# Kernel tuning notes

Hardware: AMD Instinct MI355X
Metric: run time of the kernel (lower is better)

The kernel has to match this reference:

```python
import jax, jax.numpy as jnp
import numpy as np

B, S, D_MODEL, N_HEADS, HEAD_DIM = 4, 2048, 1024, 16, 64
NEG = -1e9


def apply_rope_real(x, cos_f, sin_f):
    # x: [B, H, S, D]; cos_f/sin_f: [S, D//2] broadcast over B, H
    x_even = x[..., ::2]
    x_odd = x[..., 1::2]
    out_even = x_even * cos_f - x_odd * sin_f
    out_odd = x_even * sin_f + x_odd * cos_f
    return jnp.stack([out_even, out_odd], axis=-1).reshape(x.shape)


def setup_inputs() -> dict:
    key = jax.random.key(0)
    ks = jax.random.split(key, 8)
    x = jax.random.normal(ks[0], (B, S, D_MODEL), dtype=jnp.float32)
    # RoPE tables: theta_i = 10000^{-2i/d}, angles = pos * theta
    inv_freq = 1.0 / (10000.0 ** (jnp.arange(0, HEAD_DIM, 2, dtype=jnp.float32) / HEAD_DIM))
    angles = jnp.arange(S, dtype=jnp.float32)[:, None] * inv_freq[None, :]  # [S, D/2]
    cos_freqs = jnp.cos(angles)
    sin_freqs = jnp.sin(angles)
    causal_mask = jnp.where(jnp.tril(jnp.ones((S, S), dtype=bool)), 0.0, NEG).astype(jnp.float32)
    scale = 0.02
    w_q = jax.random.normal(ks[1], (D_MODEL, D_MODEL), dtype=jnp.float32) * scale
    w_k = jax.random.normal(ks[2], (D_MODEL, D_MODEL), dtype=jnp.float32) * scale
    w_v = jax.random.normal(ks[3], (D_MODEL, D_MODEL), dtype=jnp.float32) * scale
    w_o = jax.random.normal(ks[4], (D_MODEL, D_MODEL), dtype=jnp.float32) * scale
    return {"x": x, "cos_freqs": cos_freqs, "sin_freqs": sin_freqs,
            "causal_mask": causal_mask, "w_q": w_q, "w_k": w_k, "w_v": w_v, "w_o": w_o}


def reference(x, cos_freqs, sin_freqs, causal_mask, w_q, w_k, w_v, w_o):
    batch, seq_len, _ = x.shape
    scale = 1.0 / jnp.sqrt(jnp.float32(HEAD_DIM))
    # torch Linear: y = x @ W.T
    def proj(w):
        return (x @ w.T).reshape(batch, seq_len, N_HEADS, HEAD_DIM).transpose(0, 2, 1, 3)
    q = apply_rope_real(proj(w_q), cos_freqs, sin_freqs)
    k = apply_rope_real(proj(w_k), cos_freqs, sin_freqs)
    v = proj(w_v)
    attn = jnp.einsum('bhqd,bhkd->bhqk', q, k) * scale + causal_mask
    attn = jax.nn.softmax(attn, axis=-1)
    out = jnp.einsum('bhqk,bhkd->bhqd', attn, v)
    out = out.transpose(0, 2, 1, 3).reshape(batch, seq_len, -1)
    return out @ w_o.T
```

## Files before the change

kernel.cpp:

```cpp
#include <hip/hip_runtime.h>
#include <stdint.h>

#define B_  4
#define S_  2048
#define DM_ 1024
#define NH_ 16
#define HD_ 64

typedef unsigned short ushort_t;
typedef __bf16 bf16x8 __attribute__((ext_vector_type(8)));
typedef float  floatx4 __attribute__((ext_vector_type(4)));
typedef float  floatx16 __attribute__((ext_vector_type(16)));

__device__ __forceinline__ float bf2f(ushort_t u) {
    union { unsigned int i; float f; } v; v.i = ((unsigned int)u) << 16; return v.f;
}
__device__ __forceinline__ ushort_t f2bf(float f) {
    union { float f; unsigned int i; } v; v.f = f;
    unsigned int x = v.i;
    return (ushort_t)((x + 0x7fffu + ((x >> 16) & 1u)) >> 16);
}
__device__ __forceinline__ unsigned int pack_bf16_trunc(float lo, float hi) {
    union { float f; unsigned int u; } a, b;
    a.f = lo; b.f = hi;
    return __builtin_amdgcn_perm(b.u, a.u, 0x07060302u);
}

__global__ __launch_bounds__(256) void cvt_all_kernel(
    const float* __restrict__ x,  const float* __restrict__ wq,
    const float* __restrict__ wk, const float* __restrict__ wv,
    const float* __restrict__ wo,
    ushort_t* __restrict__ xb,  ushort_t* __restrict__ wqb,
    ushort_t* __restrict__ wkb, ushort_t* __restrict__ wvb,
    ushort_t* __restrict__ wob)
{
    const int blk = blockIdx.x;
    const float* src; ushort_t* dst; int off;
    if (blk < 8192)       { src = x;  dst = xb;  off = blk; }
    else if (blk < 9216)  { src = wq; dst = wqb; off = blk - 8192; }
    else if (blk < 10240) { src = wk; dst = wkb; off = blk - 9216; }
    else if (blk < 11264) { src = wv; dst = wvb; off = blk - 10240; }
    else                  { src = wo; dst = wob; off = blk - 11264; }
    const int i = off * 256 + threadIdx.x;
    float4 v = ((const float4*)src)[i];
    ushort4 o; o.x = f2bf(v.x); o.y = f2bf(v.y); o.z = f2bf(v.z); o.w = f2bf(v.w);
    ((ushort4*)dst)[i] = o;
}

__global__ __launch_bounds__(512, 2) void gemm_bt_kernel(
    const ushort_t* __restrict__ A,
    const ushort_t* __restrict__ B0, const ushort_t* __restrict__ B1,
    const ushort_t* __restrict__ B2,
    void* __restrict__ C0, void* __restrict__ C1, void* __restrict__ C2,
    int M, int N, int K, int mode, int nz)
{
    __shared__ ushort_t As[2][16384];
    __shared__ ushort_t Bs[2][8192];

    const int lid = blockIdx.x;
    const int cpx = gridDim.x >> 3;
    const int wg  = (lid & 7) * cpx + (lid >> 3);
    const int x   = wg / (8 * nz);
    const int rr  = wg - x * (8 * nz);
    const int y   = rr & 7;
    const int z   = rr >> 3;

    const ushort_t* Bw = z == 0 ? B0 : z == 1 ? B1 : B2;
    void* Cv           = z == 0 ? C0 : z == 1 ? C1 : C2;

    const int tid  = threadIdx.x;
    const int wave = tid >> 6, lane = tid & 63;
    const int l15 = lane & 15, quad = lane >> 4;
    const int wr = wave >> 1, wc = wave & 1;
    const int mbase = x * 256;
    const int nbase = y * 128;
    const int NT = K >> 6;

    auto stageA = [&](int bt, int t, int L0) {
#pragma unroll
        for (int L = L0; L < L0 + 2; ++L) {
            const int e8  = L * 512 + tid;
            const int row = e8 >> 3, c = e8 & 7;
            const ushort_t* src = A + (size_t)(mbase + row) * K + t * 64 + ((c ^ (row & 7)) << 3);
            __builtin_amdgcn_global_load_lds(
                (const __attribute__((address_space(1))) unsigned int*)src,
                (__attribute__((address_space(3))) unsigned int*)(&As[bt][e8 * 8]), 16, 0, 0);
        }
    };
    auto stageB = [&](int bt, int t, int L) {
        const int e8  = L * 512 + tid;
        const int row = e8 >> 3, c = e8 & 7;
        const ushort_t* src = Bw + (size_t)(nbase + row) * K + t * 64 + ((c ^ (row & 7)) << 3);
        __builtin_amdgcn_global_load_lds(
            (const __attribute__((address_space(1))) unsigned int*)src,
            (__attribute__((address_space(3))) unsigned int*)(&Bs[bt][e8 * 8]), 16, 0, 0);
    };

    floatx4 acc[4][4] = {};

    stageA(0, 0, 0); stageA(0, 0, 2);
    stageB(0, 0, 0); stageB(0, 0, 1);
    if (NT > 1) {
        stageB(1, 1, 0); stageB(1, 1, 1);
        asm volatile("s_waitcnt vmcnt(2)" ::: "memory");
    } else {
        asm volatile("s_waitcnt vmcnt(0)" ::: "memory");
    }
    __builtin_amdgcn_s_barrier();

    auto do_tile = [&](int t, int bt) {
        bf16x8 a0[2][2], a1[2][2], b0[2][2], b1[2][2];
#pragma unroll
        for (int kk = 0; kk < 2; ++kk) {
#pragma unroll
            for (int f = 0; f < 2; ++f) {
                const int row = wr * 64 + f * 16 + l15;
                a0[kk][f] = *(const bf16x8*)&As[bt][row * 64 + ((((kk << 2) | quad)) ^ (l15 & 7)) * 8];
            }
#pragma unroll
            for (int g = 0; g < 2; ++g) {
                const int row = wc * 64 + g * 16 + l15;
                b0[kk][g] = *(const bf16x8*)&Bs[bt][row * 64 + ((((kk << 2) | quad)) ^ (l15 & 7)) * 8];
            }
        }
        if (t + 1 < NT) stageA(bt ^ 1, t + 1, 0);
        __builtin_amdgcn_s_barrier();
        asm volatile("s_waitcnt lgkmcnt(0)" ::: "memory");
        __builtin_amdgcn_s_setprio(1);
#pragma unroll
        for (int kk = 0; kk < 2; ++kk)
#pragma unroll
            for (int mt = 0; mt < 2; ++mt)
#pragma unroll
                for (int nt = 0; nt < 2; ++nt)
                    acc[mt][nt] = __builtin_amdgcn_mfma_f32_16x16x32_bf16(
                        a0[kk][mt], b0[kk][nt], acc[mt][nt], 0, 0, 0);
        __builtin_amdgcn_s_setprio(0);
        __builtin_amdgcn_s_barrier();

#pragma unroll
        for (int kk = 0; kk < 2; ++kk)
#pragma unroll
            for (int g = 0; g < 2; ++g) {
                const int row = wc * 64 + 32 + g * 16 + l15;
                b1[kk][g] = *(const bf16x8*)&Bs[bt][row * 64 + ((((kk << 2) | quad)) ^ (l15 & 7)) * 8];
            }
        if (t + 1 < NT) stageA(bt ^ 1, t + 1, 2);
        __builtin_amdgcn_s_barrier();
        asm volatile("s_waitcnt lgkmcnt(0)" ::: "memory");
        __builtin_amdgcn_s_setprio(1);
#pragma unroll
        for (int kk = 0; kk < 2; ++kk)
#pragma unroll
            for (int mt = 0; mt < 2; ++mt)
#pragma unroll
                for (int nt = 0; nt < 2; ++nt)
                    acc[mt][2 + nt] = __builtin_amdgcn_mfma_f32_16x16x32_bf16(
                        a0[kk][mt], b1[kk][nt], acc[mt][2 + nt], 0, 0, 0);
        __builtin_amdgcn_s_setprio(0);
        __builtin_amdgcn_s_barrier();

#pragma unroll
        for (int kk = 0; kk < 2; ++kk)
#pragma unroll
            for (int f = 0; f < 2; ++f) {
                const int row = wr * 64 + 32 + f * 16 + l15;
                a1[kk][f] = *(const bf16x8*)&As[bt][row * 64 + ((((kk << 2) | quad)) ^ (l15 & 7)) * 8];
            }
        if (t + 2 < NT) stageB(bt, t + 2, 0);
        __builtin_amdgcn_s_barrier();
        asm volatile("s_waitcnt lgkmcnt(0)" ::: "memory");
        __builtin_amdgcn_s_setprio(1);
#pragma unroll
        for (int kk = 0; kk < 2; ++kk)
#pragma unroll
            for (int mt = 0; mt < 2; ++mt)
#pragma unroll
                for (int nt = 0; nt < 2; ++nt)
                    acc[2 + mt][2 + nt] = __builtin_amdgcn_mfma_f32_16x16x32_bf16(
                        a1[kk][mt], b1[kk][nt], acc[2 + mt][2 + nt], 0, 0, 0);
        __builtin_amdgcn_s_setprio(0);
        __builtin_amdgcn_s_barrier();

        if (t + 2 < NT) stageB(bt, t + 2, 1);
        __builtin_amdgcn_s_barrier();
        __builtin_amdgcn_s_setprio(1);
#pragma unroll
        for (int kk = 0; kk < 2; ++kk)
#pragma unroll
            for (int mt = 0; mt < 2; ++mt)
#pragma unroll
                for (int nt = 0; nt < 2; ++nt)
                    acc[2 + mt][nt] = __builtin_amdgcn_mfma_f32_16x16x32_bf16(
                        a1[kk][mt], b0[kk][nt], acc[2 + mt][nt], 0, 0, 0);
        __builtin_amdgcn_s_setprio(0);
        if (t + 2 < NT) { asm volatile("s_waitcnt vmcnt(2)" ::: "memory"); }
        else            { asm volatile("s_waitcnt vmcnt(0)" ::: "memory"); }
        __builtin_amdgcn_s_barrier();
    };

    for (int t = 0; t < NT; t += 2) {
        do_tile(t, 0);
        do_tile(t + 1, 1);
    }

    const bool vtmode = (mode == 0) && (z == 2);
#pragma unroll
    for (int mt = 0; mt < 4; ++mt) {
#pragma unroll
        for (int nt = 0; nt < 4; ++nt) {
            const int col = nbase + wc * 64 + nt * 16 + l15;
            const int m0  = mbase + wr * 64 + mt * 16 + quad * 4;
            if (vtmode) {
                const int b = m0 >> 11, s = m0 & 2047;
                const int hh = col >> 6, d = col & 63;
                uint2 pk;
                pk.x = (unsigned)f2bf(acc[mt][nt][0]) | ((unsigned)f2bf(acc[mt][nt][1]) << 16);
                pk.y = (unsigned)f2bf(acc[mt][nt][2]) | ((unsigned)f2bf(acc[mt][nt][3]) << 16);
                *(uint2*)&((ushort_t*)Cv)[((size_t)((b * NH_ + hh) * HD_ + d)) * S_ + s] = pk;
            } else if (mode == 0) {
#pragma unroll
                for (int r = 0; r < 4; ++r) {
                    const int m = m0 + r;
                    const int b = m >> 11, s = m & 2047;
                    const int hh = col >> 6, d = col & 63;
                    ((ushort_t*)Cv)[(((size_t)(b * NH_ + hh)) * S_ + s) * HD_ + d] =
                        f2bf(acc[mt][nt][r]);
                }
            } else {
#pragma unroll
                for (int r = 0; r < 4; ++r)
                    ((float*)Cv)[(size_t)(m0 + r) * N + col] = acc[mt][nt][r];
            }
        }
    }
}

#define QSCALE 0.1803368801f
__global__ __launch_bounds__(256) void rope_kernel(
    ushort_t* __restrict__ q, ushort_t* __restrict__ k,
    const float* __restrict__ cf, const float* __restrict__ sf)
{
    const int idx = blockIdx.x * 256 + threadIdx.x;
    const int j = idx & 31;
    const int s = (idx >> 5) & (S_ - 1);
    const float c  = cf[s * 32 + j];
    const float sn = sf[s * 32 + j];
    const size_t base = (size_t)idx * 2;
    float qe = bf2f(q[base]), qo = bf2f(q[base + 1]);
    q[base]     = f2bf((qe * c - qo * sn) * QSCALE);
    q[base + 1] = f2bf((qe * sn + qo * c) * QSCALE);
    float ke = bf2f(k[base]), ko = bf2f(k[base + 1]);
    k[base]     = f2bf(ke * c - ko * sn);
    k[base + 1] = f2bf(ke * sn + ko * c);
}

__global__ __launch_bounds__(256, 4) void attn_kernel(
    const ushort_t* __restrict__ Qg, const ushort_t* __restrict__ Kg,
    const ushort_t* __restrict__ Vg, ushort_t* __restrict__ Og)
{
    __shared__ ushort_t Ks[2][64 * 64];
    __shared__ ushort_t Vt[2][64 * 64];

    const int id   = blockIdx.x;
    const int sg   = id >> 3;
    const int bh   = (id & 7) * 8 + (sg & 7);
    const int qtile = 15 - (sg >> 3);
    const int tid  = threadIdx.x;
    const int wave = tid >> 6, lane = tid & 63;
    const int l31 = lane & 31, h = lane >> 5;

    const size_t bh_off = (size_t)bh * S_ * HD_;
    const int b_out = bh >> 4, h_out = bh & 15;

    const int e0 = tid, e1 = tid + 256;
    const int r0 = e0 >> 3, c0 = (e0 & 7) ^ (r0 & 7);
    const int r1 = e1 >> 3, c1 = (e1 & 7) ^ (r1 & 7);

    const int qbase = qtile * 128;
    const int nkt   = 2 * qtile + 2;
    const int qrow  = qbase + wave * 32 + l31;

    bf16x8 qf[4];
#pragma unroll
    for (int ks = 0; ks < 4; ++ks)
        qf[ks] = *(const bf16x8*)(Qg + bh_off + (size_t)qrow * HD_ + ks * 16 + h * 8);

    float m_run = -1e30f, l_run = 0.f;
    floatx16 o_acc[2] = {};

    {
        const ushort_t* ka = Kg + bh_off + (size_t)r0 * HD_ + c0 * 8;
        const ushort_t* kb = Kg + bh_off + (size_t)r1 * HD_ + c1 * 8;
        const ushort_t* va = Vg + bh_off + (size_t)r0 * S_ + c0 * 8;
        const ushort_t* vb = Vg + bh_off + (size_t)r1 * S_ + c1 * 8;
        __builtin_amdgcn_global_load_lds(
            (const __attribute__((address_space(1))) unsigned int*)ka,
            (__attribute__((address_space(3))) unsigned int*)(&Ks[0][e0 * 8]), 16, 0, 0);
        __builtin_amdgcn_global_load_lds(
            (const __attribute__((address_space(1))) unsigned int*)kb,
            (__attribute__((address_space(3))) unsigned int*)(&Ks[0][e1 * 8]), 16, 0, 0);
        __builtin_amdgcn_global_load_lds(
            (const __attribute__((address_space(1))) unsigned int*)va,
            (__attribute__((address_space(3))) unsigned int*)(&Vt[0][e0 * 8]), 16, 0, 0);
        __builtin_amdgcn_global_load_lds(
            (const __attribute__((address_space(1))) unsigned int*)vb,
            (__attribute__((address_space(3))) unsigned int*)(&Vt[0][e1 * 8]), 16, 0, 0);
    }
    asm volatile("s_waitcnt vmcnt(0)" ::: "memory");
    __syncthreads();

    for (int kt = 0; kt < nkt; ++kt) {
        const int kbase = kt * 64;
        const int cur = kt & 1;

        if (kt + 1 < nkt) {
            const int nb = kbase + 64;
            const ushort_t* ka = Kg + bh_off + (size_t)(nb + r0) * HD_ + c0 * 8;
            const ushort_t* kb = Kg + bh_off + (size_t)(nb + r1) * HD_ + c1 * 8;
            const ushort_t* va = Vg + bh_off + (size_t)r0 * S_ + nb + c0 * 8;
            const ushort_t* vb = Vg + bh_off + (size_t)r1 * S_ + nb + c1 * 8;
            __builtin_amdgcn_global_load_lds(
                (const __attribute__((address_space(1))) unsigned int*)ka,
                (__attribute__((address_space(3))) unsigned int*)(&Ks[cur ^ 1][e0 * 8]), 16, 0, 0);
            __builtin_amdgcn_global_load_lds(
                (const __attribute__((address_space(1))) unsigned int*)kb,
                (__attribute__((address_space(3))) unsigned int*)(&Ks[cur ^ 1][e1 * 8]), 16, 0, 0);
            __builtin_amdgcn_global_load_lds(
                (const __attribute__((address_space(1))) unsigned int*)va,
                (__attribute__((address_space(3))) unsigned int*)(&Vt[cur ^ 1][e0 * 8]), 16, 0, 0);
            __builtin_amdgcn_global_load_lds(
                (const __attribute__((address_space(1))) unsigned int*)vb,
                (__attribute__((address_space(3))) unsigned int*)(&Vt[cur ^ 1][e1 * 8]), 16, 0, 0);
        }

        if (kbase <= qbase + wave * 32 + 31) {
            floatx16 st[2] = {};
#pragma unroll
            for (int nt = 0; nt < 2; ++nt) {
                const int krow = nt * 32 + l31;
#pragma unroll
                for (int ks = 0; ks < 4; ++ks) {
                    bf16x8 kf = *(const bf16x8*)&Ks[cur][krow * 64 +
                                    (((ks * 2 + h) ^ (l31 & 7)) << 3)];
                    st[nt] = __builtin_amdgcn_mfma_f32_32x32x16_bf16(kf, qf[ks], st[nt], 0, 0, 0);
                }
            }
            if (kbase + 63 > qbase + wave * 32) {
#pragma unroll
                for (int nt = 0; nt < 2; ++nt) {
                    const int key0 = kbase + nt * 32 + 4 * h;
#pragma unroll
                    for (int c = 0; c < 4; ++c)
#pragma unroll
                        for (int r = 0; r < 4; ++r)
                            if (key0 + 8 * c + r > qrow) st[nt][c * 4 + r] = -1e9f;
                }
            }
            float mx = st[0][0];
#pragma unroll
            for (int nt = 0; nt < 2; ++nt)
#pragma unroll
                for (int i = 0; i < 16; ++i) mx = fmaxf(mx, st[nt][i]);
            mx = fmaxf(mx, __shfl_xor(mx, 32, 64));
            if (!__all(mx <= m_run + 8.0f)) {
                const float mnew = fmaxf(m_run, mx);
                const float alpha = __builtin_amdgcn_exp2f(m_run - mnew);
                m_run = mnew;
                l_run *= alpha;
#pragma unroll
                for (int dt = 0; dt < 2; ++dt)
#pragma unroll
                    for (int i = 0; i < 16; ++i) o_acc[dt][i] *= alpha;
            }
            float sum = 0.f;
#pragma unroll
            for (int nt = 0; nt < 2; ++nt)
#pragma unroll
                for (int i = 0; i < 16; ++i) {
                    const float p = __builtin_amdgcn_exp2f(st[nt][i] - m_run);
                    st[nt][i] = p; sum += p;
                }
            sum += __shfl_xor(sum, 32, 64);
            l_run += sum;

            bf16x8 pf[4];
#pragma unroll
            for (int ks = 0; ks < 4; ++ks) {
                const int nt = ks >> 1, base = (ks & 1) * 8;
                unsigned wrd[4];
#pragma unroll
                for (int d8 = 0; d8 < 2; ++d8) {
                    unsigned p = pack_bf16_trunc(st[nt][base + 2 * d8],
                                                 st[nt][base + 2 * d8 + 1]);
                    unsigned q = pack_bf16_trunc(st[nt][base + 4 + 2 * d8],
                                                 st[nt][base + 4 + 2 * d8 + 1]);
                    auto r = __builtin_amdgcn_permlane32_swap((int)p, (int)q, false, false);
                    wrd[d8]     = (unsigned)r[0];
                    wrd[2 + d8] = (unsigned)r[1];
                }
                union { unsigned u[4]; bf16x8 v; } cvt;
                cvt.u[0] = wrd[0]; cvt.u[1] = wrd[1];
                cvt.u[2] = wrd[2]; cvt.u[3] = wrd[3];
                pf[ks] = cvt.v;
            }

#pragma unroll
            for (int dt = 0; dt < 2; ++dt) {
                const int d = dt * 32 + l31;
#pragma unroll
                for (int ks = 0; ks < 4; ++ks) {
                    bf16x8 vf = *(const bf16x8*)&Vt[cur][d * 64 +
                                    (((ks * 2 + h) ^ (l31 & 7)) << 3)];
                    o_acc[dt] = __builtin_amdgcn_mfma_f32_32x32x16_bf16(vf, pf[ks], o_acc[dt], 0, 0, 0);
                }
            }
        }

        asm volatile("s_waitcnt vmcnt(0)" ::: "memory");
        __syncthreads();
    }

    const float inv = 1.0f / l_run;
    ushort_t* orow = Og + ((size_t)(b_out * S_ + qrow)) * DM_ + h_out * HD_;
#pragma unroll
    for (int dt = 0; dt < 2; ++dt)
#pragma unroll
        for (int c = 0; c < 4; ++c) {
            uint2 pk;
            pk.x = (unsigned)f2bf(o_acc[dt][c * 4 + 0] * inv) |
                   ((unsigned)f2bf(o_acc[dt][c * 4 + 1] * inv) << 16);
            pk.y = (unsigned)f2bf(o_acc[dt][c * 4 + 2] * inv) |
                   ((unsigned)f2bf(o_acc[dt][c * 4 + 3] * inv) << 16);
            *(uint2*)(orow + dt * 32 + 8 * c + 4 * h) = pk;
        }
}

extern "C" void kernel_launch(void* const* d_in, const int* in_sizes, int n_in,
                              void* d_out, int out_size, void* d_ws, size_t ws_size,
                              hipStream_t stream)
{
    const float* x  = (const float*)d_in[0];
    const float* cf = (const float*)d_in[1];
    const float* sf = (const float*)d_in[2];
    const float* wq = (const float*)d_in[4];
    const float* wk = (const float*)d_in[5];
    const float* wv = (const float*)d_in[6];
    const float* wo = (const float*)d_in[7];
    float* out = (float*)d_out;

    const size_t NELEM = (size_t)B_ * S_ * DM_;
    const size_t WELEM = (size_t)DM_ * DM_;
    ushort_t* xb  = (ushort_t*)d_ws;
    ushort_t* qb  = xb + NELEM;
    ushort_t* kb  = qb + NELEM;
    ushort_t* vb  = kb + NELEM;
    ushort_t* ao  = vb + NELEM;
    ushort_t* wqb = ao + NELEM;
    ushort_t* wkb = wqb + WELEM;
    ushort_t* wvb = wkb + WELEM;
    ushort_t* wob = wvb + WELEM;

    cvt_all_kernel<<<dim3(8192 + 4 * 1024), 256, 0, stream>>>(
        x, wq, wk, wv, wo, xb, wqb, wkb, wvb, wob);

    const int M = B_ * S_;
    gemm_bt_kernel<<<dim3(32 * 8 * 3), 512, 0, stream>>>(
        xb, wqb, wkb, wvb, qb, kb, vb, M, DM_, DM_, 0, 3);
    rope_kernel<<<dim3((B_ * NH_ * S_ * 32) / 256), 256, 0, stream>>>(qb, kb, cf, sf);
    attn_kernel<<<dim3(1024), 256, 0, stream>>>(qb, kb, vb, ao);
    gemm_bt_kernel<<<dim3(32 * 8), 512, 0, stream>>>(
        ao, wob, wob, wob, out, out, out, M, DM_, DM_, 1, 1);
}
```

Before: 272.1 us.

## Fuse RoPE into QKV GEMM epilogue and shrink GEMM tile to 128x128

Removes the separate RoPE kernel by applying the rotation and Q scaling inside the QKV projection GEMM epilogue, using a lane-xor shuffle to fetch the paired even/odd element. This drops one full read-modify-write pass over Q and K in global memory and one kernel launch. The GEMM also changes from 512-thread 256x128 tiles to 256-thread 128x128 tiles with a simpler two-phase pipeline per K tile, doubling the grid. The smaller tile lowers per-block data reuse in exchange for more blocks and occupancy. The epilogue now issues scattered cos/sin loads.

```diff
diff --git a/kernel.cpp b/kernel.cpp
--- a/kernel.cpp
+++ b/kernel.cpp
@@ -25,6 +25,8 @@
     a.f = lo; b.f = hi;
     return __builtin_amdgcn_perm(b.u, a.u, 0x07060302u);
 }
+
+#define QSCALE 0.1803368801f
 
 __global__ __launch_bounds__(256) void cvt_all_kernel(
     const float* __restrict__ x,  const float* __restrict__ wq,
@@ -47,14 +49,15 @@
     ((ushort4*)dst)[i] = o;
 }
 
-__global__ __launch_bounds__(512, 2) void gemm_bt_kernel(
+__global__ __launch_bounds__(256, 2) void gemm_bt_kernel(
     const ushort_t* __restrict__ A,
     const ushort_t* __restrict__ B0, const ushort_t* __restrict__ B1,
     const ushort_t* __restrict__ B2,
     void* __restrict__ C0, void* __restrict__ C1, void* __restrict__ C2,
+    const float* __restrict__ cf, const float* __restrict__ sf,
     int M, int N, int K, int mode, int nz)
 {
-    __shared__ ushort_t As[2][16384];
+    __shared__ ushort_t As[2][8192];
     __shared__ ushort_t Bs[2][8192];
 
     const int lid = blockIdx.x;
@@ -72,44 +75,49 @@
     const int wave = tid >> 6, lane = tid & 63;
     const int l15 = lane & 15, quad = lane >> 4;
     const int wr = wave >> 1, wc = wave & 1;
-    const int mbase = x * 256;
+    const int mbase = x * 128;
     const int nbase = y * 128;
     const int NT = K >> 6;
 
-    auto stageA = [&](int bt, int t, int L0) {
-#pragma unroll
-        for (int L = L0; L < L0 + 2; ++L) {
-            const int e8  = L * 512 + tid;
-            const int row = e8 >> 3, c = e8 & 7;
+    auto stageA = [&](int bt, int t) {
+#pragma unroll
+        for (int L = 0; L < 4; ++L) {
+            const int e   = L * 256 + tid;
+            const int row = e >> 3, c = e & 7;
             const ushort_t* src = A + (size_t)(mbase + row) * K + t * 64 + ((c ^ (row & 7)) << 3);
             __builtin_amdgcn_global_load_lds(
                 (const __attribute__((address_space(1))) unsigned int*)src,
-                (__attribute__((address_space(3))) unsigned int*)(&As[bt][e8 * 8]), 16, 0, 0);
+                (__attribute__((address_space(3))) unsigned int*)(&As[bt][e * 8]), 16, 0, 0);
         }
     };
-    auto stageB = [&](int bt, int t, int L) {
-        const int e8  = L * 512 + tid;
-        const int row = e8 >> 3, c = e8 & 7;
-        const ushort_t* src = Bw + (size_t)(nbase + row) * K + t * 64 + ((c ^ (row & 7)) << 3);
-        __builtin_amdgcn_global_load_lds(
-            (const __attribute__((address_space(1))) unsigned int*)src,
-            (__attribute__((address_space(3))) unsigned int*)(&Bs[bt][e8 * 8]), 16, 0, 0);
+    auto stageB = [&](int bt, int t) {
+#pragma unroll
+        for (int L = 0; L < 4; ++L) {
+            const int e   = L * 256 + tid;
+            const int row = e >> 3, c = e & 7;
+            const ushort_t* src = Bw + (size_t)(nbase + row) * K + t * 64 + ((c ^ (row & 7)) << 3);
+            __builtin_amdgcn_global_load_lds(
+                (const __attribute__((address_space(1))) unsigned int*)src,
+                (__attribute__((address_space(3))) unsigned int*)(&Bs[bt][e * 8]), 16, 0, 0);
+        }
     };
 
     floatx4 acc[4][4] = {};
 
-    stageA(0, 0, 0); stageA(0, 0, 2);
-    stageB(0, 0, 0); stageB(0, 0, 1);
+    stageA(0, 0);
+    stageB(0, 0);
     if (NT > 1) {
-        stageB(1, 1, 0); stageB(1, 1, 1);
-        asm volatile("s_waitcnt vmcnt(2)" ::: "memory");
+        stageB(1, 1);
+        asm volatile("s_waitcnt vmcnt(4)" ::: "memory");
     } else {
         asm volatile("s_waitcnt vmcnt(0)" ::: "memory");
     }
     __builtin_amdgcn_s_barrier();
 
-    auto do_tile = [&](int t, int bt) {
-        bf16x8 a0[2][2], a1[2][2], b0[2][2], b1[2][2];
+    for (int t = 0; t < NT; ++t) {
+        const int bt = t & 1;
+        bf16x8 a0[2][2], a1[2][2], bf[2][4];
+
 #pragma unroll
         for (int kk = 0; kk < 2; ++kk) {
 #pragma unroll
@@ -118,12 +126,13 @@
                 a0[kk][f] = *(const bf16x8*)&As[bt][row * 64 + ((((kk << 2) | quad)) ^ (l15 & 7)) * 8];
             }
 #pragma unroll
-            for (int g = 0; g < 2; ++g) {
+            for (int g = 0; g < 4; ++g) {
                 const int row = wc * 64 + g * 16 + l15;
-                b0[kk][g] = *(const bf16x8*)&Bs[bt][row * 64 + ((((kk << 2) | quad)) ^ (l15 & 7)) * 8];
-            }
-        }
-        if (t + 1 < NT) stageA(bt ^ 1, t + 1, 0);
+                bf[kk][g] = *(const bf16x8*)&Bs[bt][row * 64 + ((((kk << 2) | quad)) ^ (l15 & 7)) * 8];
+            }
+        }
+        if (t + 1 < NT) stageA(bt ^ 1, t + 1);
+        asm volatile("s_waitcnt lgkmcnt(8)" ::: "memory");
         __builtin_amdgcn_s_barrier();
         asm volatile("s_waitcnt lgkmcnt(0)" ::: "memory");
         __builtin_amdgcn_s_setprio(1);
@@ -132,20 +141,20 @@
 #pragma unroll
             for (int mt = 0; mt < 2; ++mt)
 #pragma unroll
-                for (int nt = 0; nt < 2; ++nt)
+                for (int nt = 0; nt < 4; ++nt)
                     acc[mt][nt] = __builtin_amdgcn_mfma_f32_16x16x32_bf16(
-                        a0[kk][mt], b0[kk][nt], acc[mt][nt], 0, 0, 0);
+                        a0[kk][mt], bf[kk][nt], acc[mt][nt], 0, 0, 0);
         __builtin_amdgcn_s_setprio(0);
         __builtin_amdgcn_s_barrier();
 
 #pragma unroll
         for (int kk = 0; kk < 2; ++kk)
 #pragma unroll
-            for (int g = 0; g < 2; ++g) {
-                const int row = wc * 64 + 32 + g * 16 + l15;
-                b1[kk][g] = *(const bf16x8*)&Bs[bt][row * 64 + ((((kk << 2) | quad)) ^ (l15 & 7)) * 8];
-            }
-        if (t + 1 < NT) stageA(bt ^ 1, t + 1, 2);
+            for (int f = 0; f < 2; ++f) {
+                const int row = wr * 64 + 32 + f * 16 + l15;
+                a1[kk][f] = *(const bf16x8*)&As[bt][row * 64 + ((((kk << 2) | quad)) ^ (l15 & 7)) * 8];
+            }
+        if (t + 2 < NT) stageB(bt, t + 2);
         __builtin_amdgcn_s_barrier();
         asm volatile("s_waitcnt lgkmcnt(0)" ::: "memory");
         __builtin_amdgcn_s_setprio(1);
@@ -154,57 +163,18 @@
 #pragma unroll
             for (int mt = 0; mt < 2; ++mt)
 #pragma unroll
-                for (int nt = 0; nt < 2; ++nt)
-                    acc[mt][2 + nt] = __builtin_amdgcn_mfma_f32_16x16x32_bf16(
-                        a0[kk][mt], b1[kk][nt], acc[mt][2 + nt], 0, 0, 0);
+                for (int nt = 0; nt < 4; ++nt)
+                    acc[2 + mt][nt] = __builtin_amdgcn_mfma_f32_16x16x32_bf16(
+                        a1[kk][mt], bf[kk][nt], acc[2 + mt][nt], 0, 0, 0);
         __builtin_amdgcn_s_setprio(0);
-        __builtin_amdgcn_s_barrier();
-
-#pragma unroll
-        for (int kk = 0; kk < 2; ++kk)
-#pragma unroll
-            for (int f = 0; f < 2; ++f) {
-                const int row = wr * 64 + 32 + f * 16 + l15;
-                a1[kk][f] = *(const bf16x8*)&As[bt][row * 64 + ((((kk << 2) | quad)) ^ (l15 & 7)) * 8];
-            }
-        if (t + 2 < NT) stageB(bt, t + 2, 0);
-        __builtin_amdgcn_s_barrier();
-        asm volatile("s_waitcnt lgkmcnt(0)" ::: "memory");
-        __builtin_amdgcn_s_setprio(1);
-#pragma unroll
-        for (int kk = 0; kk < 2; ++kk)
-#pragma unroll
-            for (int mt = 0; mt < 2; ++mt)
-#pragma unroll
-                for (int nt = 0; nt < 2; ++nt)
-                    acc[2 + mt][2 + nt] = __builtin_amdgcn_mfma_f32_16x16x32_bf16(
-                        a1[kk][mt], b1[kk][nt], acc[2 + mt][2 + nt], 0, 0, 0);
-        __builtin_amdgcn_s_setprio(0);
-        __builtin_amdgcn_s_barrier();
-
-        if (t + 2 < NT) stageB(bt, t + 2, 1);
-        __builtin_amdgcn_s_barrier();
-        __builtin_amdgcn_s_setprio(1);
-#pragma unroll
-        for (int kk = 0; kk < 2; ++kk)
-#pragma unroll
-            for (int mt = 0; mt < 2; ++mt)
-#pragma unroll
-                for (int nt = 0; nt < 2; ++nt)
-                    acc[2 + mt][nt] = __builtin_amdgcn_mfma_f32_16x16x32_bf16(
-                        a1[kk][mt], b0[kk][nt], acc[2 + mt][nt], 0, 0, 0);
-        __builtin_amdgcn_s_setprio(0);
-        if (t + 2 < NT) { asm volatile("s_waitcnt vmcnt(2)" ::: "memory"); }
+        if (t + 2 < NT) { asm volatile("s_waitcnt vmcnt(4)" ::: "memory"); }
         else            { asm volatile("s_waitcnt vmcnt(0)" ::: "memory"); }
         __builtin_amdgcn_s_barrier();
-    };
-
-    for (int t = 0; t < NT; t += 2) {
-        do_tile(t, 0);
-        do_tile(t + 1, 1);
     }
 
     const bool vtmode = (mode == 0) && (z == 2);
+    const bool ropem  = (mode == 0) && (z < 2);
+    const float qs    = (z == 0) ? QSCALE : 1.0f;
 #pragma unroll
     for (int mt = 0; mt < 4; ++mt) {
 #pragma unroll
@@ -218,14 +188,20 @@
                 pk.x = (unsigned)f2bf(acc[mt][nt][0]) | ((unsigned)f2bf(acc[mt][nt][1]) << 16);
                 pk.y = (unsigned)f2bf(acc[mt][nt][2]) | ((unsigned)f2bf(acc[mt][nt][3]) << 16);
                 *(uint2*)&((ushort_t*)Cv)[((size_t)((b * NH_ + hh) * HD_ + d)) * S_ + s] = pk;
-            } else if (mode == 0) {
+            } else if (ropem) {
+                const int d = col & 63, j = d >> 1;
+                const int hh = col >> 6;
+                const float sgn = (l15 & 1) ? 1.0f : -1.0f;
 #pragma unroll
                 for (int r = 0; r < 4; ++r) {
                     const int m = m0 + r;
                     const int b = m >> 11, s = m & 2047;
-                    const int hh = col >> 6, d = col & 63;
+                    const float v = acc[mt][nt][r];
+                    const float p = __shfl_xor(v, 1, 64);
+                    const float c  = cf[s * 32 + j] * qs;
+                    const float sn = sf[s * 32 + j] * qs * sgn;
                     ((ushort_t*)Cv)[(((size_t)(b * NH_ + hh)) * S_ + s) * HD_ + d] =
-                        f2bf(acc[mt][nt][r]);
+                        f2bf(v * c + p * sn);
                 }
             } else {
 #pragma unroll
@@ -234,25 +210,6 @@
             }
         }
     }
-}
-
-#define QSCALE 0.1803368801f
-__global__ __launch_bounds__(256) void rope_kernel(
-    ushort_t* __restrict__ q, ushort_t* __restrict__ k,
-    const float* __restrict__ cf, const float* __restrict__ sf)
-{
-    const int idx = blockIdx.x * 256 + threadIdx.x;
-    const int j = idx & 31;
-    const int s = (idx >> 5) & (S_ - 1);
-    const float c  = cf[s * 32 + j];
-    const float sn = sf[s * 32 + j];
-    const size_t base = (size_t)idx * 2;
-    float qe = bf2f(q[base]), qo = bf2f(q[base + 1]);
-    q[base]     = f2bf((qe * c - qo * sn) * QSCALE);
-    q[base + 1] = f2bf((qe * sn + qo * c) * QSCALE);
-    float ke = bf2f(k[base]), ko = bf2f(k[base + 1]);
-    k[base]     = f2bf(ke * c - ko * sn);
-    k[base + 1] = f2bf(ke * sn + ko * c);
 }
 
 __global__ __launch_bounds__(256, 4) void attn_kernel(
@@ -465,10 +422,9 @@
         x, wq, wk, wv, wo, xb, wqb, wkb, wvb, wob);
 
     const int M = B_ * S_;
-    gemm_bt_kernel<<<dim3(32 * 8 * 3), 512, 0, stream>>>(
-        xb, wqb, wkb, wvb, qb, kb, vb, M, DM_, DM_, 0, 3);
-    rope_kernel<<<dim3((B_ * NH_ * S_ * 32) / 256), 256, 0, stream>>>(qb, kb, cf, sf);
+    gemm_bt_kernel<<<dim3(64 * 8 * 3), 256, 0, stream>>>(
+        xb, wqb, wkb, wvb, qb, kb, vb, cf, sf, M, DM_, DM_, 0, 3);
     attn_kernel<<<dim3(1024), 256, 0, stream>>>(qb, kb, vb, ao);
-    gemm_bt_kernel<<<dim3(32 * 8), 512, 0, stream>>>(
-        ao, wob, wob, wob, out, out, out, M, DM_, DM_, 1, 1);
-}
+    gemm_bt_kernel<<<dim3(64 * 8), 256, 0, stream>>>(
+        ao, wob, wob, wob, out, out, out, cf, sf, M, DM_, DM_, 1, 1);
+}
```

New measurement: 254.3 us. 1.07x faster.

## Fuse RoPE into QKV GEMM epilogue and add smaller-tile output projection GEMM

Applied to the files above, without the earlier changes.

Applies RoPE and the Q scaling inside the QKV GEMM epilogue, using a lane shuffle to fetch the paired even/odd element. This removes the separate rope kernel and its read/write pass over Q and K. The output projection now uses a dedicated 128x128-tile, 256-thread GEMM with 512 blocks instead of 256 large-tile blocks, to fill more CUs. The trade-off is more cos/sin table loads in the epilogue, plus rounding to bf16 after the rotation rather than before it.

```diff
diff --git a/kernel.cpp b/kernel.cpp
--- a/kernel.cpp
+++ b/kernel.cpp
@@ -25,6 +25,8 @@
     a.f = lo; b.f = hi;
     return __builtin_amdgcn_perm(b.u, a.u, 0x07060302u);
 }
+
+#define QSCALE 0.1803368801f
 
 __global__ __launch_bounds__(256) void cvt_all_kernel(
     const float* __restrict__ x,  const float* __restrict__ wq,
@@ -47,12 +49,13 @@
     ((ushort4*)dst)[i] = o;
 }
 
-__global__ __launch_bounds__(512, 2) void gemm_bt_kernel(
+__global__ __launch_bounds__(512, 2) void gemm_qkv_kernel(
     const ushort_t* __restrict__ A,
     const ushort_t* __restrict__ B0, const ushort_t* __restrict__ B1,
     const ushort_t* __restrict__ B2,
     void* __restrict__ C0, void* __restrict__ C1, void* __restrict__ C2,
-    int M, int N, int K, int mode, int nz)
+    const float* __restrict__ cf, const float* __restrict__ sf,
+    int M, int N, int K, int nz)
 {
     __shared__ ushort_t As[2][16384];
     __shared__ ushort_t Bs[2][8192];
@@ -204,55 +207,165 @@
         do_tile(t + 1, 1);
     }
 
-    const bool vtmode = (mode == 0) && (z == 2);
+    const float qs = (z == 0) ? QSCALE : 1.0f;
 #pragma unroll
     for (int mt = 0; mt < 4; ++mt) {
 #pragma unroll
         for (int nt = 0; nt < 4; ++nt) {
             const int col = nbase + wc * 64 + nt * 16 + l15;
             const int m0  = mbase + wr * 64 + mt * 16 + quad * 4;
-            if (vtmode) {
+            if (z == 2) {
                 const int b = m0 >> 11, s = m0 & 2047;
                 const int hh = col >> 6, d = col & 63;
                 uint2 pk;
                 pk.x = (unsigned)f2bf(acc[mt][nt][0]) | ((unsigned)f2bf(acc[mt][nt][1]) << 16);
                 pk.y = (unsigned)f2bf(acc[mt][nt][2]) | ((unsigned)f2bf(acc[mt][nt][3]) << 16);
                 *(uint2*)&((ushort_t*)Cv)[((size_t)((b * NH_ + hh) * HD_ + d)) * S_ + s] = pk;
-            } else if (mode == 0) {
+            } else {
+                const int d = col & 63, j = d >> 1;
+                const int hh = col >> 6;
+                const float sgn = (l15 & 1) ? 1.0f : -1.0f;
 #pragma unroll
                 for (int r = 0; r < 4; ++r) {
                     const int m = m0 + r;
                     const int b = m >> 11, s = m & 2047;
-                    const int hh = col >> 6, d = col & 63;
+                    const float v = acc[mt][nt][r];
+                    const float p = __shfl_xor(v, 1, 64);
+                    const float c  = cf[s * 32 + j] * qs;
+                    const float sn = sf[s * 32 + j] * qs * sgn;
                     ((ushort_t*)Cv)[(((size_t)(b * NH_ + hh)) * S_ + s) * HD_ + d] =
-                        f2bf(acc[mt][nt][r]);
+                        f2bf(v * c + p * sn);
                 }
-            } else {
-#pragma unroll
-                for (int r = 0; r < 4; ++r)
-                    ((float*)Cv)[(size_t)(m0 + r) * N + col] = acc[mt][nt][r];
-            }
-        }
-    }
-}
-
-#define QSCALE 0.1803368801f
-__global__ __launch_bounds__(256) void rope_kernel(
-    ushort_t* __restrict__ q, ushort_t* __restrict__ k,
-    const float* __restrict__ cf, const float* __restrict__ sf)
+            }
+        }
+    }
+}
+
+__global__ __launch_bounds__(256, 2) void gemm_proj_kernel(
+    const ushort_t* __restrict__ A, const ushort_t* __restrict__ Bw,
+    float* __restrict__ Cv, int M, int N, int K)
 {
-    const int idx = blockIdx.x * 256 + threadIdx.x;
-    const int j = idx & 31;
-    const int s = (idx >> 5) & (S_ - 1);
-    const float c  = cf[s * 32 + j];
-    const float sn = sf[s * 32 + j];
-    const size_t base = (size_t)idx * 2;
-    float qe = bf2f(q[base]), qo = bf2f(q[base + 1]);
-    q[base]     = f2bf((qe * c - qo * sn) * QSCALE);
-    q[base + 1] = f2bf((qe * sn + qo * c) * QSCALE);
-    float ke = bf2f(k[base]), ko = bf2f(k[base + 1]);
-    k[base]     = f2bf(ke * c - ko * sn);
-    k[base + 1] = f2bf(ke * sn + ko * c);
+    __shared__ ushort_t As[2][8192];
+    __shared__ ushort_t Bs[2][8192];
+
+    const int lid = blockIdx.x;
+    const int cpx = gridDim.x >> 3;
+    const int wg  = (lid & 7) * cpx + (lid >> 3);
+    const int x   = wg >> 3;
+    const int y   = wg & 7;
+
+    const int tid  = threadIdx.x;
+    const int wave = tid >> 6, lane = tid & 63;
+    const int l15 = lane & 15, quad = lane >> 4;
+    const int wr = wave >> 1, wc = wave & 1;
+    const int mbase = x * 128;
+    const int nbase = y * 128;
+    const int NT = K >> 6;
+
+    auto stageA = [&](int bt, int t) {
+#pragma unroll
+        for (int L = 0; L < 4; ++L) {
+            const int e   = L * 256 + tid;
+            const int row = e >> 3, c = e & 7;
+            const ushort_t* src = A + (size_t)(mbase + row) * K + t * 64 + ((c ^ (row & 7)) << 3);
+            __builtin_amdgcn_global_load_lds(
+                (const __attribute__((address_space(1))) unsigned int*)src,
+                (__attribute__((address_space(3))) unsigned int*)(&As[bt][e * 8]), 16, 0, 0);
+        }
+    };
+    auto stageB = [&](int bt, int t) {
+#pragma unroll
+        for (int L = 0; L < 4; ++L) {
+            const int e   = L * 256 + tid;
+            const int row = e >> 3, c = e & 7;
+            const ushort_t* src = Bw + (size_t)(nbase + row) * K + t * 64 + ((c ^ (row & 7)) << 3);
+            __builtin_amdgcn_global_load_lds(
+                (const __attribute__((address_space(1))) unsigned int*)src,
+                (__attribute__((address_space(3))) unsigned int*)(&Bs[bt][e * 8]), 16, 0, 0);
+        }
+    };
+
+    floatx4 acc[4][4] = {};
+
+    stageA(0, 0);
+    stageB(0, 0);
+    if (NT > 1) {
+        stageB(1, 1);
+        asm volatile("s_waitcnt vmcnt(4)" ::: "memory");
+    } else {
+        asm volatile("s_waitcnt vmcnt(0)" ::: "memory");
+    }
+    __builtin_amdgcn_s_barrier();
+
+    for (int t = 0; t < NT; ++t) {
+        const int bt = t & 1;
+        bf16x8 a0[2][2], a1[2][2], bf[2][4];
+
+#pragma unroll
+        for (int kk = 0; kk < 2; ++kk) {
+#pragma unroll
+            for (int f = 0; f < 2; ++f) {
+                const int row = wr * 64 + f * 16 + l15;
+                a0[kk][f] = *(const bf16x8*)&As[bt][row * 64 + ((((kk << 2) | quad)) ^ (l15 & 7)) * 8];
+            }
+#pragma unroll
+            for (int g = 0; g < 4; ++g) {
+                const int row = wc * 64 + g * 16 + l15;
+                bf[kk][g] = *(const bf16x8*)&Bs[bt][row * 64 + ((((kk << 2) | quad)) ^ (l15 & 7)) * 8];
+            }
+        }
+        if (t + 1 < NT) stageA(bt ^ 1, t + 1);
+        asm volatile("s_waitcnt lgkmcnt(8)" ::: "memory");
+        __builtin_amdgcn_s_barrier();
+        asm volatile("s_waitcnt lgkmcnt(0)" ::: "memory");
+        __builtin_amdgcn_s_setprio(1);
+#pragma unroll
+        for (int kk = 0; kk < 2; ++kk)
+#pragma unroll
+            for (int mt = 0; mt < 2; ++mt)
+#pragma unroll
+                for (int nt = 0; nt < 4; ++nt)
+                    acc[mt][nt] = __builtin_amdgcn_mfma_f32_16x16x32_bf16(
+                        a0[kk][mt], bf[kk][nt], acc[mt][nt], 0, 0, 0);
+        __builtin_amdgcn_s_setprio(0);
+        __builtin_amdgcn_s_barrier();
+
+#pragma unroll
+        for (int kk = 0; kk < 2; ++kk)
+#pragma unroll
+            for (int f = 0; f < 2; ++f) {
+                const int row = wr * 64 + 32 + f * 16 + l15;
+                a1[kk][f] = *(const bf16x8*)&As[bt][row * 64 + ((((kk << 2) | quad)) ^ (l15 & 7)) * 8];
+            }
+        if (t + 2 < NT) stageB(bt, t + 2);
+        __builtin_amdgcn_s_barrier();
+        asm volatile("s_waitcnt lgkmcnt(0)" ::: "memory");
+        __builtin_amdgcn_s_setprio(1);
+#pragma unroll
+        for (int kk = 0; kk < 2; ++kk)
+#pragma unroll
+            for (int mt = 0; mt < 2; ++mt)
+#pragma unroll
+                for (int nt = 0; nt < 4; ++nt)
+                    acc[2 + mt][nt] = __builtin_amdgcn_mfma_f32_16x16x32_bf16(
+                        a1[kk][mt], bf[kk][nt], acc[2 + mt][nt], 0, 0, 0);
+        __builtin_amdgcn_s_setprio(0);
+        if (t + 2 < NT) { asm volatile("s_waitcnt vmcnt(4)" ::: "memory"); }
+        else            { asm volatile("s_waitcnt vmcnt(0)" ::: "memory"); }
+        __builtin_amdgcn_s_barrier();
+    }
+
+#pragma unroll
+    for (int mt = 0; mt < 4; ++mt) {
+#pragma unroll
+        for (int nt = 0; nt < 4; ++nt) {
+            const int col = nbase + wc * 64 + nt * 16 + l15;
+            const int m0  = mbase + wr * 64 + mt * 16 + quad * 4;
+#pragma unroll
+            for (int r = 0; r < 4; ++r)
+                Cv[(size_t)(m0 + r) * N + col] = acc[mt][nt][r];
+        }
+    }
 }
 
 __global__ __launch_bounds__(256, 4) void attn_kernel(
@@ -465,10 +578,9 @@
         x, wq, wk, wv, wo, xb, wqb, wkb, wvb, wob);
 
     const int M = B_ * S_;
-    gemm_bt_kernel<<<dim3(32 * 8 * 3), 512, 0, stream>>>(
-        xb, wqb, wkb, wvb, qb, kb, vb, M, DM_, DM_, 0, 3);
-    rope_kernel<<<dim3((B_ * NH_ * S_ * 32) / 256), 256, 0, stream>>>(qb, kb, cf, sf);
+    gemm_qkv_kernel<<<dim3(32 * 8 * 3), 512, 0, stream>>>(
+        xb, wqb, wkb, wvb, qb, kb, vb, cf, sf, M, DM_, DM_, 3);
     attn_kernel<<<dim3(1024), 256, 0, stream>>>(qb, kb, vb, ao);
-    gemm_bt_kernel<<<dim3(32 * 8), 512, 0, stream>>>(
-        ao, wob, wob, wob, out, out, out, M, DM_, DM_, 1, 1);
-}
+    gemm_proj_kernel<<<dim3(64 * 8), 256, 0, stream>>>(
+        ao, wob, out, M, DM_, DM_);
+}
```

After: 259.3 us. 1.05x faster.
